# Kernel tuning notes

Measured on AMD Instinct MI355X. Metric: run time of the kernel, lower is better.

The kernel has to match this reference:

```python
import jax, jax.numpy as jnp
import numpy as np

N = 1024          # number of junctions
H = 1024          # heatmap height
W = 1024          # heatmap width
NUM_SAMPLES = 64  # samples along each candidate segment (torch_sampler)
DETECT_THRESH = 0.5
INLIER_THRESH = 0.99


def setup_inputs() -> dict:
    key = jax.random.key(0)
    k1, k2 = jax.random.split(key)
    # junctions are (h, w) float coordinates inside the image
    junctions = jax.random.uniform(k1, (N, 2), dtype=jnp.float32) * (H - 1)
    heatmap = jax.random.uniform(k2, (H, W), dtype=jnp.float32)
    return {"junctions": junctions, "heatmap": heatmap}


def _bilinear_sample(heatmap, ch, cw):
    """SOLD2 detect_bilinear: gather 4 corners, bilinear weights. ch/cw: [N,N,S]."""
    hf = jnp.floor(ch); hc = jnp.ceil(ch)
    wf = jnp.floor(cw); wc = jnp.ceil(cw)
    hfi = hf.astype(jnp.int32); hci = hc.astype(jnp.int32)
    wfi = wf.astype(jnp.int32); wci = wc.astype(jnp.int32)
    return (heatmap[hfi, wfi] * (hc - ch) * (wc - cw)
          + heatmap[hfi, wci] * (hc - ch) * (cw - wf)
          + heatmap[hci, wfi] * (ch - hf) * (wc - cw)
          + heatmap[hci, wci] * (ch - hf) * (cw - wf))


def reference(junctions, heatmap):
    n = junctions.shape[0]
    Hh, Ww = heatmap.shape
    t = jnp.linspace(0.0, 1.0, NUM_SAMPLES, dtype=jnp.float32)  # [S]
    # cand_samples[i, j, s] = junc[i] * t[s] + junc[j] * (1 - t[s])  (start=i, end=j)
    ch = junctions[:, None, 0:1] * t + junctions[None, :, 0:1] * (1.0 - t)  # [N,N,S]
    cw = junctions[:, None, 1:2] * t + junctions[None, :, 1:2] * (1.0 - t)  # [N,N,S]
    ch = jnp.clip(ch, 0.0, Hh - 1)
    cw = jnp.clip(cw, 0.0, Ww - 1)
    feat = _bilinear_sample(heatmap, ch, cw)                    # [N,N,S]
    mean_feat = feat.mean(axis=-1)                              # [N,N]
    inlier_ratio = (feat > DETECT_THRESH).astype(jnp.float32).mean(axis=-1)
    # candidate map: strict upper triangle (torch.triu(ones, diagonal=1))
    cand_mask = jnp.triu(jnp.ones((n, n), dtype=bool), k=1)
    detected = (mean_feat > DETECT_THRESH) & (inlier_ratio >= INLIER_THRESH) & cand_mask
    line_map = (detected | detected.T).astype(jnp.int32)        # symmetric line map
    return line_map, mean_feat
```

## Files before the change

kernel.cpp:

```cpp
#include <hip/hip_runtime.h>

#define NJ 1024
#define DETECT 0.5f
#define RESCUE 0.4975f

__device__ __forceinline__ float sample_t(int s) {
    return (s == 63) ? 1.0f : (float)s * (1.0f / 63.0f);
}

__device__ __forceinline__ void exact_pair(const float2 ja, const float2 jb,
                                           const float* __restrict__ heat,
                                           float& mean_o, float& min_o)
{
    float acc = 0.0f;
    float mn  = __builtin_inff();
    for (int s = 0; s < 64; ++s) {
        const float t  = sample_t(s);
        const float om = 1.0f - t;
        float ch = __fadd_rn(__fmul_rn(ja.x, t), __fmul_rn(jb.x, om));
        float cw = __fadd_rn(__fmul_rn(ja.y, t), __fmul_rn(jb.y, om));
        ch = fminf(fmaxf(ch, 0.0f), 1023.0f);
        cw = fminf(fmaxf(cw, 0.0f), 1023.0f);
        const float hf = floorf(ch), hc = ceilf(ch);
        const float wf = floorf(cw), wc = ceilf(cw);
        const int hfi = (int)hf, hci = (int)hc;
        const int wfi = (int)wf, wci = (int)wc;
        const float a00 = heat[(hfi << 10) + wfi];
        const float a01 = heat[(hfi << 10) + wci];
        const float a10 = heat[(hci << 10) + wfi];
        const float a11 = heat[(hci << 10) + wci];
        const float t1 = __fmul_rn(__fmul_rn(a00, __fsub_rn(hc, ch)), __fsub_rn(wc, cw));
        const float t2 = __fmul_rn(__fmul_rn(a01, __fsub_rn(hc, ch)), __fsub_rn(cw, wf));
        const float t3 = __fmul_rn(__fmul_rn(a10, __fsub_rn(ch, hf)), __fsub_rn(wc, cw));
        const float t4 = __fmul_rn(__fmul_rn(a11, __fsub_rn(ch, hf)), __fsub_rn(cw, wf));
        const float feat = __fadd_rn(__fadd_rn(__fadd_rn(t1, t2), t3), t4);
        acc += feat;
        mn = fminf(mn, feat);
    }
    mean_o = acc * (1.0f / 64.0f);
    min_o  = mn;
}

__global__ __launch_bounds__(256) void pack_kernel(
    const float* __restrict__ heat, uint4* __restrict__ packed4)
{
    const int idx = blockIdx.x * 256 + threadIdx.x;
    const int h = idx >> 8;
    const int w4 = (idx & 255) << 2;
    const int hn = (h < 1023) ? h + 1 : 1023;
    const float* r0 = heat + (h  << 10);
    const float* r1 = heat + (hn << 10);
    const float4 a = *(const float4*)(r0 + w4);
    const float4 b = *(const float4*)(r1 + w4);
    const int wnext = (w4 + 4 <= 1023) ? w4 + 4 : 1023;
    const float a4 = r0[wnext];
    const float b4 = r1[wnext];

    const float av[5] = {a.x, a.y, a.z, a.w, a4};
    const float bv[5] = {b.x, b.y, b.z, b.w, b4};
    unsigned int out[4];
    #pragma unroll
    for (int u = 0; u < 4; ++u) {
        const unsigned int c0 = (unsigned int)__float2int_rn(av[u]     * 255.0f);
        const unsigned int c1 = (unsigned int)__float2int_rn(av[u + 1] * 255.0f);
        const unsigned int c2 = (unsigned int)__float2int_rn(bv[u]     * 255.0f);
        const unsigned int c3 = (unsigned int)__float2int_rn(bv[u + 1] * 255.0f);
        out[u] = c0 | (c1 << 8) | (c2 << 16) | (c3 << 24);
    }
    packed4[idx] = make_uint4(out[0], out[1], out[2], out[3]);
}

__device__ __forceinline__ unsigned int expand_bits16(unsigned int v) {
    v &= 0x0000FFFFu;
    v = (v | (v << 8)) & 0x00FF00FFu;
    v = (v | (v << 4)) & 0x0F0F0F0Fu;
    v = (v | (v << 2)) & 0x33333333u;
    v = (v | (v << 1)) & 0x55555555u;
    return v;
}

__global__ __launch_bounds__(1024) void sort_kernel(
    const float* __restrict__ junc, float2* __restrict__ sortedJ,
    int* __restrict__ perm)
{
    __shared__ unsigned int sk[1024];
    __shared__ unsigned short sv[1024];
    const int t = threadIdx.x;
    const float2 jc = ((const float2*)junc)[t];
    const int mh = min(max((int)jc.x, 0), 1023);
    const int mw = min(max((int)jc.y, 0), 1023);
    sk[t] = (expand_bits16((unsigned int)mh) << 1) | expand_bits16((unsigned int)mw);
    sv[t] = (unsigned short)t;
    __syncthreads();

    for (unsigned int k = 2; k <= 1024; k <<= 1) {
        for (unsigned int s = k >> 1; s > 0; s >>= 1) {
            const int l = t ^ (int)s;
            if (l > t) {
                const unsigned int a = sk[t], b = sk[l];
                const bool up = ((t & k) == 0);
                if ((a > b) == up) {
                    sk[t] = b; sk[l] = a;
                    const unsigned short va = sv[t];
                    sv[t] = sv[l]; sv[l] = va;
                }
            }
            __syncthreads();
        }
    }
    const int src = (int)sv[t];
    perm[t] = src;
    sortedJ[t] = ((const float2*)junc)[src];
}

__global__ __launch_bounds__(256) void sold2_thread_kernel(
    const float2* __restrict__ sortedJ,
    const int* __restrict__ perm,
    const float* __restrict__ heat,
    const unsigned int* __restrict__ packed,
    float* __restrict__ line_out,
    float* __restrict__ mean_out)
{
    const int q = blockIdx.x * 256 + threadIdx.x;
    const int r = q / 513;
    const int c = q - r * 513;
    const int jc = (r + c) & 1023;

    const float2 jr = sortedJ[r];
    const float2 jj = sortedJ[jc];

    float acc = 0.0f;
    float mn  = __builtin_inff();

    #pragma unroll
    for (int s0 = 0; s0 < 64; s0 += 16) {
        float chv[16], cwv[16];
        unsigned int cv[16];
        #pragma unroll
        for (int u = 0; u < 16; ++u) {
            const int s = s0 + u;
            const float t  = sample_t(s);
            const float om = 1.0f - t;
            float ch = __fadd_rn(__fmul_rn(jr.x, t), __fmul_rn(jj.x, om));
            float cw = __fadd_rn(__fmul_rn(jr.y, t), __fmul_rn(jj.y, om));
            ch = fminf(fmaxf(ch, 0.0f), 1023.0f);
            cw = fminf(fmaxf(cw, 0.0f), 1023.0f);
            chv[u] = ch;
            cwv[u] = cw;
            const int hfi = (int)ch;
            const int wfi = (int)cw;
            cv[u] = packed[(hfi << 10) + wfi];
        }
        #pragma unroll
        for (int u = 0; u < 16; ++u) {
            const float ch = chv[u], cw = cwv[u];
            const float hf = floorf(ch), hc = ceilf(ch);
            const float wf = floorf(cw), wc = ceilf(cw);
            const float wh0 = hc - ch, wh1 = ch - hf;
            const float ww0 = wc - cw, ww1 = cw - wf;
            const unsigned int cc = cv[u];
            const float a00 = (float)(cc & 0xffu);
            const float a01 = (float)((cc >> 8) & 0xffu);
            const float a10 = (float)((cc >> 16) & 0xffu);
            const float a11 = (float)(cc >> 24);
            const float feat = a00 * (wh0 * ww0) + a01 * (wh0 * ww1)
                             + a10 * (wh1 * ww0) + a11 * (wh1 * ww1);
            acc += feat;
            mn = fminf(mn, feat);
        }
    }

    float mean = acc * (1.0f / (255.0f * 64.0f));
    const float mns = mn * (1.0f / 255.0f);

    bool det = false;
    if ((mns > RESCUE) && (mean > RESCUE) && (c != 0)) {
        float mn2;
        exact_pair(jr, jj, heat, mean, mn2);
        det = (mean > DETECT) && (mn2 > DETECT);
    }

    const int io = perm[r];
    const int jo = perm[jc];
    const float lv = det ? 1.0f : 0.0f;

    const int p1 = (io << 10) + jo;
    __builtin_nontemporal_store(mean, mean_out + p1);
    __builtin_nontemporal_store(lv,   line_out + p1);

    if (c != 0 && c != 512) {
        const int p2 = (jo << 10) + io;
        __builtin_nontemporal_store(mean, mean_out + p2);
        __builtin_nontemporal_store(lv,   line_out + p2);
    }
}

extern "C" void kernel_launch(void* const* d_in, const int* in_sizes, int n_in,
                              void* d_out, int out_size, void* d_ws, size_t ws_size,
                              hipStream_t stream) {
    const float* junc = (const float*)d_in[0];
    const float* heat = (const float*)d_in[1];
    float* line_out = (float*)d_out;
    float* mean_out = line_out + NJ * NJ;

    unsigned int* packed = (unsigned int*)d_ws;
    float2* sortedJ = (float2*)((char*)d_ws + (4u << 20));
    int* perm = (int*)((char*)d_ws + (4u << 20) + 8192);

    pack_kernel<<<1024, 256, 0, stream>>>(heat, (uint4*)packed);
    sort_kernel<<<1, 1024, 0, stream>>>(junc, sortedJ, perm);

    const int total = NJ * 513;
    sold2_thread_kernel<<<total / 256, 256, 0, stream>>>(sortedJ, perm, heat,
                                                         packed, line_out, mean_out);
}
```

Baseline: 181.5 us.

## Tile packed heatmap 4x4, fuse prep kernels, move diagonal to prep

Stores the packed 8-bit bilinear-corner heatmap in 4x4 tiles so that nearby samples along a segment fall in the same cache lines. Merges the pack and sort kernels into one launch, with the sort done by 256 threads handling four elements each. Diagonal pairs move into extra prep blocks, so the main kernel drops its division by 513 and works on a power-of-two grid. The cost is address swizzling on every gather and a sort run by fewer threads.

Measured after the change: 186.7 us. 2.9% more time.

```diff
diff --git a/kernel.cpp b/kernel.cpp
--- a/kernel.cpp
+++ b/kernel.cpp
@@ -6,6 +6,10 @@
 
 __device__ __forceinline__ float sample_t(int s) {
     return (s == 63) ? 1.0f : (float)s * (1.0f / 63.0f);
+}
+
+__device__ __forceinline__ int tiled_idx(int h, int w) {
+    return ((h >> 2) << 12) + ((w >> 2) << 4) + ((h & 3) << 2) + (w & 3);
 }
 
 __device__ __forceinline__ void exact_pair(const float2 ja, const float2 jb,
@@ -41,35 +45,6 @@
     min_o  = mn;
 }
 
-__global__ __launch_bounds__(256) void pack_kernel(
-    const float* __restrict__ heat, uint4* __restrict__ packed4)
-{
-    const int idx = blockIdx.x * 256 + threadIdx.x;
-    const int h = idx >> 8;
-    const int w4 = (idx & 255) << 2;
-    const int hn = (h < 1023) ? h + 1 : 1023;
-    const float* r0 = heat + (h  << 10);
-    const float* r1 = heat + (hn << 10);
-    const float4 a = *(const float4*)(r0 + w4);
-    const float4 b = *(const float4*)(r1 + w4);
-    const int wnext = (w4 + 4 <= 1023) ? w4 + 4 : 1023;
-    const float a4 = r0[wnext];
-    const float b4 = r1[wnext];
-
-    const float av[5] = {a.x, a.y, a.z, a.w, a4};
-    const float bv[5] = {b.x, b.y, b.z, b.w, b4};
-    unsigned int out[4];
-    #pragma unroll
-    for (int u = 0; u < 4; ++u) {
-        const unsigned int c0 = (unsigned int)__float2int_rn(av[u]     * 255.0f);
-        const unsigned int c1 = (unsigned int)__float2int_rn(av[u + 1] * 255.0f);
-        const unsigned int c2 = (unsigned int)__float2int_rn(bv[u]     * 255.0f);
-        const unsigned int c3 = (unsigned int)__float2int_rn(bv[u + 1] * 255.0f);
-        out[u] = c0 | (c1 << 8) | (c2 << 16) | (c3 << 24);
-    }
-    packed4[idx] = make_uint4(out[0], out[1], out[2], out[3]);
-}
-
 __device__ __forceinline__ unsigned int expand_bits16(unsigned int v) {
     v &= 0x0000FFFFu;
     v = (v | (v << 8)) & 0x00FF00FFu;
@@ -79,38 +54,88 @@
     return v;
 }
 
-__global__ __launch_bounds__(1024) void sort_kernel(
-    const float* __restrict__ junc, float2* __restrict__ sortedJ,
-    int* __restrict__ perm)
+__global__ __launch_bounds__(256) void prep_kernel(
+    const float* __restrict__ junc, const float* __restrict__ heat,
+    unsigned int* __restrict__ packed, float2* __restrict__ sortedJ,
+    int* __restrict__ perm, float* __restrict__ line_out,
+    float* __restrict__ mean_out)
 {
-    __shared__ unsigned int sk[1024];
-    __shared__ unsigned short sv[1024];
-    const int t = threadIdx.x;
-    const float2 jc = ((const float2*)junc)[t];
-    const int mh = min(max((int)jc.x, 0), 1023);
-    const int mw = min(max((int)jc.y, 0), 1023);
-    sk[t] = (expand_bits16((unsigned int)mh) << 1) | expand_bits16((unsigned int)mw);
-    sv[t] = (unsigned short)t;
-    __syncthreads();
-
-    for (unsigned int k = 2; k <= 1024; k <<= 1) {
-        for (unsigned int s = k >> 1; s > 0; s >>= 1) {
-            const int l = t ^ (int)s;
-            if (l > t) {
-                const unsigned int a = sk[t], b = sk[l];
-                const bool up = ((t & k) == 0);
-                if ((a > b) == up) {
-                    sk[t] = b; sk[l] = a;
-                    const unsigned short va = sv[t];
-                    sv[t] = sv[l]; sv[l] = va;
+    const int b = blockIdx.x;
+    if (b < 1024) {
+        const int idx = b * 256 + threadIdx.x;
+        const int h = idx >> 8;
+        const int w4 = (idx & 255) << 2;
+        const int hn = (h < 1023) ? h + 1 : 1023;
+        const float* r0 = heat + (h  << 10);
+        const float* r1 = heat + (hn << 10);
+        const float4 a = *(const float4*)(r0 + w4);
+        const float4 bq = *(const float4*)(r1 + w4);
+        const int wnext = (w4 + 4 <= 1023) ? w4 + 4 : 1023;
+        const float a4 = r0[wnext];
+        const float b4 = r1[wnext];
+
+        const float av[5] = {a.x, a.y, a.z, a.w, a4};
+        const float bv[5] = {bq.x, bq.y, bq.z, bq.w, b4};
+        unsigned int out[4];
+        #pragma unroll
+        for (int u = 0; u < 4; ++u) {
+            const unsigned int c0 = (unsigned int)__float2int_rn(av[u]     * 255.0f);
+            const unsigned int c1 = (unsigned int)__float2int_rn(av[u + 1] * 255.0f);
+            const unsigned int c2 = (unsigned int)__float2int_rn(bv[u]     * 255.0f);
+            const unsigned int c3 = (unsigned int)__float2int_rn(bv[u]     * 0.0f
+                                   + bv[u + 1] * 255.0f);
+            out[u] = c0 | (c1 << 8) | (c2 << 16) | (c3 << 24);
+        }
+        *(uint4*)(packed + tiled_idx(h, w4)) = make_uint4(out[0], out[1], out[2], out[3]);
+    } else if (b == 1024) {
+        __shared__ unsigned int   sk[1024];
+        __shared__ unsigned short sv[1024];
+        const int t = threadIdx.x;
+        #pragma unroll
+        for (int m = 0; m < 4; ++m) {
+            const int i = (m << 8) + t;
+            const float2 jc2 = ((const float2*)junc)[i];
+            const int mh = min(max((int)jc2.x, 0), 1023);
+            const int mw = min(max((int)jc2.y, 0), 1023);
+            sk[i] = (expand_bits16((unsigned int)mh) << 1)
+                  |  expand_bits16((unsigned int)mw);
+            sv[i] = (unsigned short)i;
+        }
+        __syncthreads();
+        for (unsigned int k = 2; k <= 1024; k <<= 1) {
+            for (unsigned int s = k >> 1; s > 0; s >>= 1) {
+                #pragma unroll
+                for (int m = 0; m < 4; ++m) {
+                    const int i = (m << 8) + t;
+                    const int l = i ^ (int)s;
+                    if (l > i) {
+                        const unsigned int ka = sk[i], kb = sk[l];
+                        const bool up = ((i & (int)k) == 0);
+                        if ((ka > kb) == up) {
+                            sk[i] = kb; sk[l] = ka;
+                            const unsigned short va = sv[i];
+                            sv[i] = sv[l]; sv[l] = va;
+                        }
+                    }
                 }
+                __syncthreads();
             }
-            __syncthreads();
-        }
-    }
-    const int src = (int)sv[t];
-    perm[t] = src;
-    sortedJ[t] = ((const float2*)junc)[src];
+        }
+        #pragma unroll
+        for (int m = 0; m < 4; ++m) {
+            const int i = (m << 8) + t;
+            const int src = (int)sv[i];
+            perm[i] = src;
+            sortedJ[i] = ((const float2*)junc)[src];
+        }
+    } else {
+        const int i = ((b - 1025) << 8) + threadIdx.x;
+        const float2 ji = ((const float2*)junc)[i];
+        float mean, mn;
+        exact_pair(ji, ji, heat, mean, mn);
+        mean_out[(i << 10) + i] = mean;
+        line_out[(i << 10) + i] = 0.0f;
+    }
 }
 
 __global__ __launch_bounds__(256) void sold2_thread_kernel(
@@ -122,8 +147,8 @@
     float* __restrict__ mean_out)
 {
     const int q = blockIdx.x * 256 + threadIdx.x;
-    const int r = q / 513;
-    const int c = q - r * 513;
+    const int r = q >> 9;
+    const int c = 1 + (q & 511);
     const int jc = (r + c) & 1023;
 
     const float2 jr = sortedJ[r];
@@ -149,7 +174,7 @@
             cwv[u] = cw;
             const int hfi = (int)ch;
             const int wfi = (int)cw;
-            cv[u] = packed[(hfi << 10) + wfi];
+            cv[u] = packed[tiled_idx(hfi, wfi)];
         }
         #pragma unroll
         for (int u = 0; u < 16; ++u) {
@@ -174,7 +199,7 @@
     const float mns = mn * (1.0f / 255.0f);
 
     bool det = false;
-    if ((mns > RESCUE) && (mean > RESCUE) && (c != 0)) {
+    if ((mns > RESCUE) && (mean > RESCUE)) {
         float mn2;
         exact_pair(jr, jj, heat, mean, mn2);
         det = (mean > DETECT) && (mn2 > DETECT);
@@ -188,7 +213,7 @@
     __builtin_nontemporal_store(mean, mean_out + p1);
     __builtin_nontemporal_store(lv,   line_out + p1);
 
-    if (c != 0 && c != 512) {
+    if (c != 512) {
         const int p2 = (jo << 10) + io;
         __builtin_nontemporal_store(mean, mean_out + p2);
         __builtin_nontemporal_store(lv,   line_out + p2);
@@ -207,10 +232,10 @@
     float2* sortedJ = (float2*)((char*)d_ws + (4u << 20));
     int* perm = (int*)((char*)d_ws + (4u << 20) + 8192);
 
-    pack_kernel<<<1024, 256, 0, stream>>>(heat, (uint4*)packed);
-    sort_kernel<<<1, 1024, 0, stream>>>(junc, sortedJ, perm);
-
-    const int total = NJ * 513;
+    prep_kernel<<<1029, 256, 0, stream>>>(junc, heat, packed, sortedJ, perm,
+                                          line_out, mean_out);
+
+    const int total = NJ * 512;
     sold2_thread_kernel<<<total / 256, 256, 0, stream>>>(sortedJ, perm, heat,
                                                          packed, line_out, mean_out);
 }
```
